# Kernel tuning notes

Measured on AMD Instinct MI355X. Metric: run time of the kernel, lower is better.

## Reference

```python
import jax, jax.numpy as jnp
import numpy as np

DIM = 1024
NUM_HEADS = 16
HEAD_DIM = DIM // NUM_HEADS
ROPE_BASE = 10000.0


def apply_rope(x, pos):
    """x: [B, H, N, D] float32, pos: [B, N] int -> rotated x (rotate-half convention)."""
    d = x.shape[-1]
    # inv_freq: [D/2]
    inv_freq = 1.0 / (ROPE_BASE ** (jnp.arange(0, d, 2, dtype=jnp.float32) / d))
    # angles: [B, 1, N, D/2]
    ang = pos.astype(jnp.float32)[:, None, :, None] * inv_freq
    cos = jnp.concatenate([jnp.cos(ang), jnp.cos(ang)], axis=-1)
    sin = jnp.concatenate([jnp.sin(ang), jnp.sin(ang)], axis=-1)
    x1, x2 = x[..., : d // 2], x[..., d // 2 :]
    rotated = jnp.concatenate([-x2, x1], axis=-1)
    return x * cos + rotated * sin


def setup_inputs() -> dict:
    key = jax.random.key(0)
    ks = jax.random.split(key, 10)
    B, Nq, Nk, C = 4, 512, 2048, DIM
    scale = 0.02
    inp = {
        "query": jax.random.normal(ks[0], (B, Nq, C), dtype=jnp.float32),
        "key": jax.random.normal(ks[1], (B, Nk, C), dtype=jnp.float32),
        "value": jax.random.normal(ks[2], (B, Nk, C), dtype=jnp.float32),
        "qpos": jnp.sort(jax.random.randint(ks[3], (B, Nq), 0, Nk, dtype=jnp.int32), axis=-1),
        "kpos": jnp.sort(jax.random.randint(ks[4], (B, Nk), 0, Nk, dtype=jnp.int32), axis=-1),
        # learned params (qkv_bias=False; output proj has bias, per nn.Linear default)
        "Wq": jax.random.normal(ks[5], (C, C), dtype=jnp.float32) * scale,
        "Wk": jax.random.normal(ks[6], (C, C), dtype=jnp.float32) * scale,
        "Wv": jax.random.normal(ks[7], (C, C), dtype=jnp.float32) * scale,
        "Wp": jax.random.normal(ks[8], (C, C), dtype=jnp.float32) * scale,
        "bp": jax.random.normal(ks[9], (C,), dtype=jnp.float32) * scale,
    }
    return inp


def reference(query, key, value, qpos, kpos, Wq, Wk, Wv, Wp, bp):
    B, Nq, C = query.shape
    Nk = key.shape[1]
    H, D = NUM_HEADS, C // NUM_HEADS
    scale = D ** (-0.5)

    # separate Q/K/V linear projections (bias=False), split heads -> [B, H, N, D]
    q = (query @ Wq.T).reshape(B, Nq, H, D).transpose(0, 2, 1, 3)
    k = (key @ Wk.T).reshape(B, Nk, H, D).transpose(0, 2, 1, 3)
    v = (value @ Wv.T).reshape(B, Nk, H, D).transpose(0, 2, 1, 3)

    # RoPE applied in fp32 (matches the cast-to-float/rotate/cast-back sequence)
    q = apply_rope(q.astype(jnp.float32), qpos).astype(query.dtype)
    k = apply_rope(k.astype(jnp.float32), kpos).astype(key.dtype)

    # scaled dot-product attention (dropout_p = 0.0, non-causal)
    scores = jnp.einsum("bhqd,bhkd->bhqk", q, k) * scale
    attn = jax.nn.softmax(scores, axis=-1)
    x = jnp.einsum("bhqk,bhkd->bhqd", attn, v)

    # merge heads and output projection (with bias)
    x = x.transpose(0, 2, 1, 3).reshape(B, Nq, C)
    x = x @ Wp.T + bp
    return x
```

## Files before the change

### kernel.cpp

```cpp
#include <hip/hip_runtime.h>
#include <math.h>

#define B_ 4
#define NQ 512
#define NK 2048
#define C_ 1024
#define H_ 16
#define D_ 64
#define KK 1024

typedef __attribute__((ext_vector_type(8))) _Float16 half8;
typedef __attribute__((ext_vector_type(4))) _Float16 half4;
typedef __attribute__((ext_vector_type(4))) float float4v;

__device__ __forceinline__ void g2l16(const _Float16* g, _Float16* l)
{
    __builtin_amdgcn_global_load_lds(
        (const __attribute__((address_space(1))) unsigned int*)g,
        (__attribute__((address_space(3))) unsigned int*)l, 16, 0, 0);
}

__global__ __launch_bounds__(256) void cvt_all(const float* __restrict__ W0,
                                               const float* __restrict__ W1,
                                               const float* __restrict__ W2,
                                               const float* __restrict__ W3,
                                               const float* __restrict__ q,
                                               const float* __restrict__ k,
                                               const float* __restrict__ v,
                                               _Float16* __restrict__ W16,
                                               _Float16* __restrict__ xq,
                                               _Float16* __restrict__ xk,
                                               _Float16* __restrict__ xv)
{
    const int blk = blockIdx.x;
    const float* src; _Float16* dst; int row;
    if (blk < 4096) {
        const int w = blk >> 10; row = blk & 1023;
        src = (w == 0) ? W0 : (w == 1) ? W1 : (w == 2) ? W2 : W3;
        dst = W16 + ((size_t)w << 20);
    } else {
        const int b2 = blk - 4096;
        if (b2 < 2048)       { src = q; dst = xq; row = b2; }
        else if (b2 < 10240) { src = k; dst = xk; row = b2 - 2048; }
        else                 { src = v; dst = xv; row = b2 - 10240; }
    }
    const int col = threadIdx.x * 4;
    float4 f = *(const float4*)(src + (size_t)row * 1024 + col);
    half4 h;
    h[0] = (_Float16)f.x; h[1] = (_Float16)f.y;
    h[2] = (_Float16)f.z; h[3] = (_Float16)f.w;
    *(half4*)(dst + (size_t)row * 1024 + col) = h;
}

__device__ __forceinline__ void gemm_body(const _Float16* __restrict__ A,
                                          const _Float16* __restrict__ Bw,
                                          _Float16* __restrict__ Yh,
                                          float* __restrict__ Yf,
                                          int mode, int nsh, int m0, int n0,
                                          const float* __restrict__ bias,
                                          _Float16* sA, _Float16* sB)
{
    const int tid = threadIdx.x;
    const int lane = tid & 63, wave = tid >> 6;
    const int wm = (wave >> 1) * 64, wn = (wave & 1) * 64;
    const int fm = lane & 15, quad = lane >> 4;

    const int srow = wave * 32 + (lane >> 3);
    const int soct = (lane & 7) ^ (srow & 7);
    const _Float16* gA = A  + (size_t)(m0 + srow) * KK + soct * 8;
    const _Float16* gB = Bw + (size_t)(n0 + srow) * KK + soct * 8;

    float4v acc[4][4];
    #pragma unroll
    for (int i = 0; i < 4; ++i)
        #pragma unroll
        for (int j = 0; j < 4; ++j)
            #pragma unroll
            for (int e = 0; e < 4; ++e) acc[i][j][e] = 0.0f;

    for (int k0 = 0; k0 < KK; k0 += 64) {
        __syncthreads();
        #pragma unroll
        for (int u = 0; u < 4; ++u) {
            g2l16(gA + (size_t)u * 8 * KK + k0, &sA[(wave * 32 + u * 8) * 64]);
            g2l16(gB + (size_t)u * 8 * KK + k0, &sB[(wave * 32 + u * 8) * 64]);
        }
        __syncthreads();

        #pragma unroll
        for (int ks = 0; ks < 2; ++ks) {
            const int po = ((ks * 4 + quad) ^ (fm & 7)) * 8;
            half8 a[4], b[4];
            #pragma unroll
            for (int i = 0; i < 4; ++i) {
                a[i] = *(const half8*)&sA[(wm + i * 16 + fm) * 64 + po];
                b[i] = *(const half8*)&sB[(wn + i * 16 + fm) * 64 + po];
            }
            __builtin_amdgcn_s_setprio(1);
            #pragma unroll
            for (int i = 0; i < 4; ++i)
                #pragma unroll
                for (int j = 0; j < 4; ++j)
                    acc[i][j] = __builtin_amdgcn_mfma_f32_16x16x32_f16(a[i], b[j], acc[i][j], 0, 0, 0);
            __builtin_amdgcn_s_setprio(0);
        }
    }

    const int rr = quad * 4;
    if (mode == 0) {
        const int nmask = (1 << nsh) - 1;
        #pragma unroll
        for (int i = 0; i < 4; ++i)
            #pragma unroll
            for (int r = 0; r < 4; ++r) {
                const int m = m0 + wm + i * 16 + rr + r;
                const int b = m >> nsh, n = m & nmask;
                #pragma unroll
                for (int j = 0; j < 4; ++j) {
                    const int c = n0 + wn + j * 16 + fm;
                    Yh[((((size_t)b * H_ + (c >> 6)) << nsh) + n) * 64 + (c & 63)] = (_Float16)acc[i][j][r];
                }
            }
    } else if (mode == 2) {
        const int nmask = (1 << nsh) - 1;
        #pragma unroll
        for (int i = 0; i < 4; ++i)
            #pragma unroll
            for (int r = 0; r < 4; ++r) {
                const int m = m0 + wm + i * 16 + rr + r;
                const int b = m >> nsh, n = m & nmask;
                #pragma unroll
                for (int j = 0; j < 4; ++j) {
                    const int c = n0 + wn + j * 16 + fm;
                    Yh[(((size_t)(b * H_ + (c >> 6)) * 64) + (c & 63)) * NK + n] = (_Float16)acc[i][j][r];
                }
            }
    } else {
        #pragma unroll
        for (int i = 0; i < 4; ++i)
            #pragma unroll
            for (int r = 0; r < 4; ++r) {
                const int m = m0 + wm + i * 16 + rr + r;
                #pragma unroll
                for (int j = 0; j < 4; ++j) {
                    const int c = n0 + wn + j * 16 + fm;
                    Yf[(size_t)m * 1024 + c] = acc[i][j][r] + bias[c];
                }
            }
    }
}

__global__ __launch_bounds__(256) void gemm_qkv(const _Float16* __restrict__ xq,
                                                const _Float16* __restrict__ xk,
                                                const _Float16* __restrict__ xv,
                                                const _Float16* __restrict__ W16,
                                                _Float16* __restrict__ qhp,
                                                _Float16* __restrict__ khp,
                                                _Float16* __restrict__ vtp)
{
    __shared__ _Float16 sA[128 * 64];
    __shared__ _Float16 sB[128 * 64];

    const int lbid = blockIdx.x;
    const int xcd = lbid & 7;
    const int seq = lbid >> 3;
    const int y = xcd + 8 * (seq >> 3);
    const int n0 = (seq & 7) * 128;

    if (y < 64)
        gemm_body(xk, W16 + (1u << 20), khp, nullptr, 0, 11, y * 128, n0, nullptr, sA, sB);
    else if (y < 128)
        gemm_body(xv, W16 + (2u << 20), vtp, nullptr, 2, 11, (y - 64) * 128, n0, nullptr, sA, sB);
    else
        gemm_body(xq, W16, qhp, nullptr, 0, 9, (y - 128) * 128, n0, nullptr, sA, sB);
}

__global__ __launch_bounds__(256) void gemm_out(const _Float16* __restrict__ A,
                                                const _Float16* __restrict__ Bw,
                                                float* __restrict__ Yf,
                                                const float* __restrict__ bias)
{
    __shared__ _Float16 sA[128 * 64];
    __shared__ _Float16 sB[128 * 64];
    gemm_body(A, Bw, nullptr, Yf, 1, 0, blockIdx.y * 128, blockIdx.x * 128, bias, sA, sB);
}

__global__ __launch_bounds__(256) void rope_qk(_Float16* __restrict__ qh,
                                               _Float16* __restrict__ kh,
                                               const int* __restrict__ qpos,
                                               const int* __restrict__ kpos)
{
    int idx = blockIdx.x * 256 + threadIdx.x;
    const int QTOT = B_ * H_ * NQ * 32;
    _Float16* t; const int* pos; int Nseq; float scale;
    if (idx < QTOT) { t = qh; pos = qpos; Nseq = NQ; scale = 0.125f; }
    else { idx -= QTOT; t = kh; pos = kpos; Nseq = NK; scale = 1.0f; }

    const int i = idx & 31;
    const int n = (idx >> 5) % Nseq;
    const int b = (idx / (32 * Nseq)) >> 4;

    double f = 1.0;
    if (i & 1)  f *= 0.7498942093324559;
    if (i & 2)  f *= 0.5623413251903491;
    if (i & 4)  f *= 0.31622776601683794;
    if (i & 8)  f *= 0.1;
    if (i & 16) f *= 0.01;

    const double ang = (double)pos[b * Nseq + n] * f;
    const double TWO_PI = 6.2831853071795864769;
    const double INV_TWO_PI = 0.15915494309189533577;
    const float red = (float)(ang - TWO_PI * floor(ang * INV_TWO_PI));
    float s, c;
    sincosf(red, &s, &c);

    const size_t base = ((size_t)(idx >> 5)) * 64 + i;
    const float x1 = (float)t[base];
    const float x2 = (float)t[base + 32];
    t[base]      = (_Float16)((x1 * c - x2 * s) * scale);
    t[base + 32] = (_Float16)((x2 * c + x1 * s) * scale);
}

__global__ __launch_bounds__(512) void attn_fused(const _Float16* __restrict__ qh,
                                                  const _Float16* __restrict__ kh,
                                                  const _Float16* __restrict__ vt,
                                                  _Float16* __restrict__ xw16)
{
    __shared__ _Float16 sK[2][64 * 64];
    __shared__ _Float16 sV[2][64 * 64];
    __shared__ _Float16 ps[8][16][66];

    const int tid = threadIdx.x;
    const int lane = tid & 63, wv = tid >> 6;
    const int bhi = blockIdx.x & 63;
    const int qquad = blockIdx.x >> 6;
    const size_t bh = (size_t)bhi;
    const int qt = qquad * 8 + wv;

    const int fm = lane & 15;
    const int quad = lane >> 4;
    const int fq = quad * 8;

    const _Float16* kb = kh + bh * NK * 64;
    const _Float16* vb = vt + bh * (size_t)64 * NK;

    const int r0 = lane >> 3;
    const int c4 = lane & 7;
    const int sch = c4 ^ r0;
    const _Float16* gK = kb + (size_t)(wv * 8 + r0) * 64 + sch * 8;
    const _Float16* gV = vb + (size_t)(wv * 8 + r0) * NK + sch * 8;

    const _Float16* qb = qh + (bh * NQ + (size_t)qt * 16) * 64;
    half8 aq[2];
    aq[0] = *(const half8*)(qb + (size_t)fm * 64 + fq);
    aq[1] = *(const half8*)(qb + (size_t)fm * 64 + 32 + fq);

    float l_acc[4] = {};
    float4v O[4];
    #pragma unroll
    for (int j = 0; j < 4; ++j)
        #pragma unroll
        for (int e = 0; e < 4; ++e) O[j][e] = 0.0f;

    const float4v z4 = {0.0f, 0.0f, 0.0f, 0.0f};

    g2l16(gK, &sK[0][wv * 512]);
    g2l16(gV, &sV[0][wv * 512]);
    __syncthreads();

    for (int it = 0; it < 32; ++it) {
        const int cur = it & 1;
        if (it < 31) {
            g2l16(gK + (size_t)(it + 1) * 64 * 64, &sK[cur ^ 1][wv * 512]);
            g2l16(gV + (it + 1) * 64,              &sV[cur ^ 1][wv * 512]);
        }
        const _Float16* Kc = sK[cur];
        const _Float16* Vc = sV[cur];

        half8 bk[4][2];
        #pragma unroll
        for (int j = 0; j < 4; ++j)
            #pragma unroll
            for (int ks = 0; ks < 2; ++ks)
                bk[j][ks] = *(const half8*)&Kc[(j * 16 + fm) * 64 + (((ks * 4 + quad) ^ (fm & 7)) * 8)];

        float4v s[4];
        __builtin_amdgcn_s_setprio(1);
        #pragma unroll
        for (int j = 0; j < 4; ++j) {
            s[j] = __builtin_amdgcn_mfma_f32_16x16x32_f16(aq[0], bk[j][0], z4, 0, 0, 0);
            s[j] = __builtin_amdgcn_mfma_f32_16x16x32_f16(aq[1], bk[j][1], s[j], 0, 0, 0);
        }
        __builtin_amdgcn_s_setprio(0);

        half8 bv[4][2];
        #pragma unroll
        for (int j = 0; j < 4; ++j)
            #pragma unroll
            for (int ks = 0; ks < 2; ++ks)
                bv[j][ks] = *(const half8*)&Vc[(j * 16 + fm) * 64 + (((ks * 4 + quad) ^ (fm & 7)) * 8)];

        #pragma unroll
        for (int j = 0; j < 4; ++j)
            #pragma unroll
            for (int r = 0; r < 4; ++r) {
                const float p = __expf(s[j][r]);
                l_acc[r] += p;
                ps[wv][quad * 4 + r][16 * j + fm] = (_Float16)p;
            }

        __builtin_amdgcn_s_setprio(1);
        #pragma unroll
        for (int ks = 0; ks < 2; ++ks) {
            half8 pa = *(const half8*)&ps[wv][fm][ks * 32 + fq];
            #pragma unroll
            for (int j = 0; j < 4; ++j)
                O[j] = __builtin_amdgcn_mfma_f32_16x16x32_f16(pa, bv[j][ks], O[j], 0, 0, 0);
        }
        __builtin_amdgcn_s_setprio(0);

        __syncthreads();
    }

    #pragma unroll
    for (int r = 0; r < 4; ++r) {
        float l = l_acc[r];
        l += __shfl_xor(l, 1);
        l += __shfl_xor(l, 2);
        l += __shfl_xor(l, 4);
        l += __shfl_xor(l, 8);
        const float inv = 1.0f / l;
        const int qr = quad * 4 + r;
        const int row = (bhi >> 4) * 512 + qt * 16 + qr;
        #pragma unroll
        for (int j = 0; j < 4; ++j) {
            const int col = (bhi & 15) * 64 + j * 16 + fm;
            xw16[(size_t)row * 1024 + col] = (_Float16)(O[j][r] * inv);
        }
    }
}

extern "C" void kernel_launch(void* const* d_in, const int* in_sizes, int n_in,
                              void* d_out, int out_size, void* d_ws, size_t ws_size,
                              hipStream_t stream)
{
    const float* query = (const float*)d_in[0];
    const float* key   = (const float*)d_in[1];
    const float* value = (const float*)d_in[2];
    const int*   qpos  = (const int*)d_in[3];
    const int*   kpos  = (const int*)d_in[4];
    const float* Wq    = (const float*)d_in[5];
    const float* Wk    = (const float*)d_in[6];
    const float* Wv    = (const float*)d_in[7];
    const float* Wp    = (const float*)d_in[8];
    const float* bp    = (const float*)d_in[9];
    float* out = (float*)d_out;

    char* ws = (char*)d_ws;
    _Float16* xk16  = (_Float16*)(ws);
    _Float16* xv16  = (_Float16*)(ws + (16u << 20));
    _Float16* xq16  = (_Float16*)(ws + (32u << 20));
    _Float16* W16   = (_Float16*)(ws + (36u << 20));
    _Float16* qhp   = (_Float16*)(ws + (44u << 20));
    _Float16* khp   = (_Float16*)(ws + (48u << 20));
    _Float16* vtp   = (_Float16*)(ws + (64u << 20));

    cvt_all<<<22528, 256, 0, stream>>>(Wq, Wk, Wv, Wp, query, key, value,
                                       W16, xq16, xk16, xv16);

    gemm_qkv<<<1152, 256, 0, stream>>>(xq16, xk16, xv16, W16, qhp, khp, vtp);

    rope_qk<<<(B_ * H_ * (NQ + NK) * 32) / 256, 256, 0, stream>>>(qhp, khp, qpos, kpos);

    attn_fused<<<256, 512, 0, stream>>>(qhp, khp, vtp, xq16);

    gemm_out<<<dim3(8, 16), 256, 0, stream>>>(xq16, W16 + (3u << 20), out, bp);
}
```

Measured before the change: 268.3 us.

## Fuse activation fp16 conversion and RoPE into QKV projection GEMM

Drops the separate fp32→fp16 conversion pass over query/key/value. The projection GEMM now loads fp32 activations into registers, converts them in-kernel and writes them to LDS, prefetching the next K-slice into registers. RoPE plus the query scale is applied in the GEMM epilogue using a precomputed cos/sin table indexed by position, so the standalone rope kernel and its extra read/write of Q and K are removed. The cost is more register pressure, twice the global bytes for the A operand inside the GEMM, and A staging that no longer uses direct global-to-LDS loads.

```diff
diff --git a/kernel.cpp b/kernel.cpp
--- a/kernel.cpp
+++ b/kernel.cpp
@@ -20,55 +20,80 @@
         (__attribute__((address_space(3))) unsigned int*)l, 16, 0, 0);
 }
 
-__global__ __launch_bounds__(256) void cvt_all(const float* __restrict__ W0,
-                                               const float* __restrict__ W1,
-                                               const float* __restrict__ W2,
-                                               const float* __restrict__ W3,
-                                               const float* __restrict__ q,
-                                               const float* __restrict__ k,
-                                               const float* __restrict__ v,
-                                               _Float16* __restrict__ W16,
-                                               _Float16* __restrict__ xq,
-                                               _Float16* __restrict__ xk,
-                                               _Float16* __restrict__ xv)
+__global__ __launch_bounds__(256) void cvt_w_tab(const float* __restrict__ W0,
+                                                 const float* __restrict__ W1,
+                                                 const float* __restrict__ W2,
+                                                 const float* __restrict__ W3,
+                                                 _Float16* __restrict__ W16,
+                                                 float2* __restrict__ tab)
 {
     const int blk = blockIdx.x;
-    const float* src; _Float16* dst; int row;
     if (blk < 4096) {
-        const int w = blk >> 10; row = blk & 1023;
-        src = (w == 0) ? W0 : (w == 1) ? W1 : (w == 2) ? W2 : W3;
-        dst = W16 + ((size_t)w << 20);
-    } else {
-        const int b2 = blk - 4096;
-        if (b2 < 2048)       { src = q; dst = xq; row = b2; }
-        else if (b2 < 10240) { src = k; dst = xk; row = b2 - 2048; }
-        else                 { src = v; dst = xv; row = b2 - 10240; }
-    }
-    const int col = threadIdx.x * 4;
-    float4 f = *(const float4*)(src + (size_t)row * 1024 + col);
-    half4 h;
-    h[0] = (_Float16)f.x; h[1] = (_Float16)f.y;
-    h[2] = (_Float16)f.z; h[3] = (_Float16)f.w;
-    *(half4*)(dst + (size_t)row * 1024 + col) = h;
-}
-
-__device__ __forceinline__ void gemm_body(const _Float16* __restrict__ A,
-                                          const _Float16* __restrict__ Bw,
-                                          _Float16* __restrict__ Yh,
-                                          float* __restrict__ Yf,
-                                          int mode, int nsh, int m0, int n0,
-                                          const float* __restrict__ bias,
-                                          _Float16* sA, _Float16* sB)
-{
+        const int w = blk >> 10, row = blk & 1023;
+        const float* src = (w == 0) ? W0 : (w == 1) ? W1 : (w == 2) ? W2 : W3;
+        const int col = threadIdx.x * 4;
+        float4 f = *(const float4*)(src + (size_t)row * 1024 + col);
+        half4 h;
+        h[0] = (_Float16)f.x; h[1] = (_Float16)f.y;
+        h[2] = (_Float16)f.z; h[3] = (_Float16)f.w;
+        *(half4*)(W16 + ((size_t)w << 20) + (size_t)row * 1024 + col) = h;
+        return;
+    }
+    const int idx = (blk - 4096) * 256 + threadIdx.x;
+    const int p = idx >> 5, i = idx & 31;
+
+    double f = 1.0;
+    if (i & 1)  f *= 0.7498942093324559;
+    if (i & 2)  f *= 0.5623413251903491;
+    if (i & 4)  f *= 0.31622776601683794;
+    if (i & 8)  f *= 0.1;
+    if (i & 16) f *= 0.01;
+
+    const double ang = (double)p * f;
+    const double TWO_PI = 6.2831853071795864769;
+    const double INV_TWO_PI = 0.15915494309189533577;
+    const float red = (float)(ang - TWO_PI * floor(ang * INV_TWO_PI));
+    float s, c;
+    sincosf(red, &s, &c);
+    tab[idx] = make_float2(c, s);
+}
+
+__global__ __launch_bounds__(256) void gemm_proj(const float* __restrict__ qf,
+                                                 const float* __restrict__ kf,
+                                                 const float* __restrict__ vf,
+                                                 const _Float16* __restrict__ W16,
+                                                 const int* __restrict__ qpos,
+                                                 const int* __restrict__ kpos,
+                                                 const float2* __restrict__ tab,
+                                                 _Float16* __restrict__ qhp,
+                                                 _Float16* __restrict__ khp,
+                                                 _Float16* __restrict__ vtp)
+{
+    __shared__ _Float16 sA[128 * 64];
+    __shared__ _Float16 sB[128 * 64];
+
+    const int lbid = blockIdx.x;
+    const int xcd = lbid & 7;
+    const int seq = lbid >> 3;
+    const int y = xcd + 8 * (seq >> 3);
+    const int n0 = (seq & 7) * 128;
+
+    const float* A; const _Float16* Bw; _Float16* Yh; const int* pos;
+    int nsh, m0, mode; float scale;
+    if (y < 64)       { A = kf; Bw = W16 + (1u << 20); Yh = khp; pos = kpos; nsh = 11; m0 = y * 128;         mode = 0; scale = 1.0f; }
+    else if (y < 128) { A = vf; Bw = W16 + (2u << 20); Yh = vtp; pos = nullptr; nsh = 11; m0 = (y - 64) * 128;  mode = 2; scale = 0.0f; }
+    else              { A = qf; Bw = W16;              Yh = qhp; pos = qpos; nsh = 9;  m0 = (y - 128) * 128; mode = 0; scale = 0.125f; }
+
     const int tid = threadIdx.x;
     const int lane = tid & 63, wave = tid >> 6;
     const int wm = (wave >> 1) * 64, wn = (wave & 1) * 64;
     const int fm = lane & 15, quad = lane >> 4;
 
-    const int srow = wave * 32 + (lane >> 3);
-    const int soct = (lane & 7) ^ (srow & 7);
-    const _Float16* gA = A  + (size_t)(m0 + srow) * KK + soct * 8;
-    const _Float16* gB = Bw + (size_t)(n0 + srow) * KK + soct * 8;
+    const int r0 = lane >> 3;
+    const int c4 = lane & 7;
+    const int sc = c4 ^ r0;
+    const float*    gAl = A  + (size_t)(m0 + wave * 32 + r0) * KK + sc * 8;
+    const _Float16* gB  = Bw + (size_t)(n0 + wave * 32 + r0) * KK + sc * 8;
 
     float4v acc[4][4];
     #pragma unroll
@@ -77,15 +102,37 @@
         for (int j = 0; j < 4; ++j)
             #pragma unroll
             for (int e = 0; e < 4; ++e) acc[i][j][e] = 0.0f;
+
+    float4 va[8];
+    #pragma unroll
+    for (int u = 0; u < 4; ++u) {
+        va[2 * u]     = *(const float4*)(gAl + (size_t)u * 8 * KK);
+        va[2 * u + 1] = *(const float4*)(gAl + (size_t)u * 8 * KK + 4);
+    }
 
     for (int k0 = 0; k0 < KK; k0 += 64) {
         __syncthreads();
         #pragma unroll
         for (int u = 0; u < 4; ++u) {
-            g2l16(gA + (size_t)u * 8 * KK + k0, &sA[(wave * 32 + u * 8) * 64]);
+            half8 h;
+            h[0] = (_Float16)va[2 * u].x; h[1] = (_Float16)va[2 * u].y;
+            h[2] = (_Float16)va[2 * u].z; h[3] = (_Float16)va[2 * u].w;
+            h[4] = (_Float16)va[2 * u + 1].x; h[5] = (_Float16)va[2 * u + 1].y;
+            h[6] = (_Float16)va[2 * u + 1].z; h[7] = (_Float16)va[2 * u + 1].w;
+            *(half8*)&sA[(wave * 32 + u * 8 + r0) * 64 + c4 * 8] = h;
+        }
+        #pragma unroll
+        for (int u = 0; u < 4; ++u)
             g2l16(gB + (size_t)u * 8 * KK + k0, &sB[(wave * 32 + u * 8) * 64]);
-        }
         __syncthreads();
+
+        if (k0 + 64 < KK) {
+            #pragma unroll
+            for (int u = 0; u < 4; ++u) {
+                va[2 * u]     = *(const float4*)(gAl + (size_t)u * 8 * KK + k0 + 64);
+                va[2 * u + 1] = *(const float4*)(gAl + (size_t)u * 8 * KK + k0 + 68);
+            }
+        }
 
         #pragma unroll
         for (int ks = 0; ks < 2; ++ks) {
@@ -109,19 +156,29 @@
     const int rr = quad * 4;
     if (mode == 0) {
         const int nmask = (1 << nsh) - 1;
+        const int hidx = (n0 + wn) >> 6;
         #pragma unroll
         for (int i = 0; i < 4; ++i)
             #pragma unroll
             for (int r = 0; r < 4; ++r) {
                 const int m = m0 + wm + i * 16 + rr + r;
                 const int b = m >> nsh, n = m & nmask;
-                #pragma unroll
-                for (int j = 0; j < 4; ++j) {
-                    const int c = n0 + wn + j * 16 + fm;
-                    Yh[((((size_t)b * H_ + (c >> 6)) << nsh) + n) * 64 + (c & 63)] = (_Float16)acc[i][j][r];
-                }
-            }
-    } else if (mode == 2) {
+                const int p = pos[(b << nsh) + n];
+                const float2 cs0 = tab[p * 32 + fm];
+                const float2 cs1 = tab[p * 32 + 16 + fm];
+                const float x0 = acc[i][0][r], x2 = acc[i][2][r];
+                const float x1 = acc[i][1][r], x3 = acc[i][3][r];
+                const float o0 = (x0 * cs0.x - x2 * cs0.y) * scale;
+                const float o2 = (x2 * cs0.x + x0 * cs0.y) * scale;
+                const float o1 = (x1 * cs1.x - x3 * cs1.y) * scale;
+                const float o3 = (x3 * cs1.x + x1 * cs1.y) * scale;
+                const size_t base = ((((size_t)b * H_ + hidx) << nsh) + n) * 64 + fm;
+                Yh[base +  0] = (_Float16)o0;
+                Yh[base + 16] = (_Float16)o1;
+                Yh[base + 32] = (_Float16)o2;
+                Yh[base + 48] = (_Float16)o3;
+            }
+    } else {
         const int nmask = (1 << nsh) - 1;
         #pragma unroll
         for (int i = 0; i < 4; ++i)
@@ -135,44 +192,7 @@
                     Yh[(((size_t)(b * H_ + (c >> 6)) * 64) + (c & 63)) * NK + n] = (_Float16)acc[i][j][r];
                 }
             }
-    } else {
-        #pragma unroll
-        for (int i = 0; i < 4; ++i)
-            #pragma unroll
-            for (int r = 0; r < 4; ++r) {
-                const int m = m0 + wm + i * 16 + rr + r;
-                #pragma unroll
-                for (int j = 0; j < 4; ++j) {
-                    const int c = n0 + wn + j * 16 + fm;
-                    Yf[(size_t)m * 1024 + c] = acc[i][j][r] + bias[c];
-                }
-            }
-    }
-}
-
-__global__ __launch_bounds__(256) void gemm_qkv(const _Float16* __restrict__ xq,
-                                                const _Float16* __restrict__ xk,
-                                                const _Float16* __restrict__ xv,
-                                                const _Float16* __restrict__ W16,
-                                                _Float16* __restrict__ qhp,
-                                                _Float16* __restrict__ khp,
-                                                _Float16* __restrict__ vtp)
-{
-    __shared__ _Float16 sA[128 * 64];
-    __shared__ _Float16 sB[128 * 64];
-
-    const int lbid = blockIdx.x;
-    const int xcd = lbid & 7;
-    const int seq = lbid >> 3;
-    const int y = xcd + 8 * (seq >> 3);
-    const int n0 = (seq & 7) * 128;
-
-    if (y < 64)
-        gemm_body(xk, W16 + (1u << 20), khp, nullptr, 0, 11, y * 128, n0, nullptr, sA, sB);
-    else if (y < 128)
-        gemm_body(xv, W16 + (2u << 20), vtp, nullptr, 2, 11, (y - 64) * 128, n0, nullptr, sA, sB);
-    else
-        gemm_body(xq, W16, qhp, nullptr, 0, 9, (y - 128) * 128, n0, nullptr, sA, sB);
+    }
 }
 
 __global__ __launch_bounds__(256) void gemm_out(const _Float16* __restrict__ A,
@@ -182,43 +202,66 @@
 {
     __shared__ _Float16 sA[128 * 64];
     __shared__ _Float16 sB[128 * 64];
-    gemm_body(A, Bw, nullptr, Yf, 1, 0, blockIdx.y * 128, blockIdx.x * 128, bias, sA, sB);
-}
-
-__global__ __launch_bounds__(256) void rope_qk(_Float16* __restrict__ qh,
-                                               _Float16* __restrict__ kh,
-                                               const int* __restrict__ qpos,
-                                               const int* __restrict__ kpos)
-{
-    int idx = blockIdx.x * 256 + threadIdx.x;
-    const int QTOT = B_ * H_ * NQ * 32;
-    _Float16* t; const int* pos; int Nseq; float scale;
-    if (idx < QTOT) { t = qh; pos = qpos; Nseq = NQ; scale = 0.125f; }
-    else { idx -= QTOT; t = kh; pos = kpos; Nseq = NK; scale = 1.0f; }
-
-    const int i = idx & 31;
-    const int n = (idx >> 5) % Nseq;
-    const int b = (idx / (32 * Nseq)) >> 4;
-
-    double f = 1.0;
-    if (i & 1)  f *= 0.7498942093324559;
-    if (i & 2)  f *= 0.5623413251903491;
-    if (i & 4)  f *= 0.31622776601683794;
-    if (i & 8)  f *= 0.1;
-    if (i & 16) f *= 0.01;
-
-    const double ang = (double)pos[b * Nseq + n] * f;
-    const double TWO_PI = 6.2831853071795864769;
-    const double INV_TWO_PI = 0.15915494309189533577;
-    const float red = (float)(ang - TWO_PI * floor(ang * INV_TWO_PI));
-    float s, c;
-    sincosf(red, &s, &c);
-
-    const size_t base = ((size_t)(idx >> 5)) * 64 + i;
-    const float x1 = (float)t[base];
-    const float x2 = (float)t[base + 32];
-    t[base]      = (_Float16)((x1 * c - x2 * s) * scale);
-    t[base + 32] = (_Float16)((x2 * c + x1 * s) * scale);
+
+    const int tid = threadIdx.x;
+    const int lane = tid & 63, wave = tid >> 6;
+    const int n0 = blockIdx.x * 128, m0 = blockIdx.y * 128;
+    const int wm = (wave >> 1) * 64, wn = (wave & 1) * 64;
+    const int fm = lane & 15, quad = lane >> 4;
+
+    const int srow = wave * 32 + (lane >> 3);
+    const int soct = (lane & 7) ^ (srow & 7);
+    const _Float16* gA = A  + (size_t)(m0 + srow) * KK + soct * 8;
+    const _Float16* gB = Bw + (size_t)(n0 + srow) * KK + soct * 8;
+
+    float4v acc[4][4];
+    #pragma unroll
+    for (int i = 0; i < 4; ++i)
+        #pragma unroll
+        for (int j = 0; j < 4; ++j)
+            #pragma unroll
+            for (int e = 0; e < 4; ++e) acc[i][j][e] = 0.0f;
+
+    for (int k0 = 0; k0 < KK; k0 += 64) {
+        __syncthreads();
+        #pragma unroll
+        for (int u = 0; u < 4; ++u) {
+            g2l16(gA + (size_t)u * 8 * KK + k0, &sA[(wave * 32 + u * 8) * 64]);
+            g2l16(gB + (size_t)u * 8 * KK + k0, &sB[(wave * 32 + u * 8) * 64]);
+        }
+        __syncthreads();
+
+        #pragma unroll
+        for (int ks = 0; ks < 2; ++ks) {
+            const int po = ((ks * 4 + quad) ^ (fm & 7)) * 8;
+            half8 a[4], b[4];
+            #pragma unroll
+            for (int i = 0; i < 4; ++i) {
+                a[i] = *(const half8*)&sA[(wm + i * 16 + fm) * 64 + po];
+                b[i] = *(const half8*)&sB[(wn + i * 16 + fm) * 64 + po];
+            }
+            __builtin_amdgcn_s_setprio(1);
+            #pragma unroll
+            for (int i = 0; i < 4; ++i)
+                #pragma unroll
+                for (int j = 0; j < 4; ++j)
+                    acc[i][j] = __builtin_amdgcn_mfma_f32_16x16x32_f16(a[i], b[j], acc[i][j], 0, 0, 0);
+            __builtin_amdgcn_s_setprio(0);
+        }
+    }
+
+    const int rr = quad * 4;
+    #pragma unroll
+    for (int i = 0; i < 4; ++i)
+        #pragma unroll
+        for (int r = 0; r < 4; ++r) {
+            const int m = m0 + wm + i * 16 + rr + r;
+            #pragma unroll
+            for (int j = 0; j < 4; ++j) {
+                const int c = n0 + wn + j * 16 + fm;
+                Yf[(size_t)m * 1024 + c] = acc[i][j][r] + bias[c];
+            }
+        }
 }
 
 __global__ __launch_bounds__(512) void attn_fused(const _Float16* __restrict__ qh,
@@ -357,22 +400,19 @@
     float* out = (float*)d_out;
 
     char* ws = (char*)d_ws;
-    _Float16* xk16  = (_Float16*)(ws);
-    _Float16* xv16  = (_Float16*)(ws + (16u << 20));
-    _Float16* xq16  = (_Float16*)(ws + (32u << 20));
+    float2*   tab   = (float2*)  (ws);
+    _Float16* xw16  = (_Float16*)(ws + (32u << 20));
     _Float16* W16   = (_Float16*)(ws + (36u << 20));
     _Float16* qhp   = (_Float16*)(ws + (44u << 20));
     _Float16* khp   = (_Float16*)(ws + (48u << 20));
     _Float16* vtp   = (_Float16*)(ws + (64u << 20));
 
-    cvt_all<<<22528, 256, 0, stream>>>(Wq, Wk, Wv, Wp, query, key, value,
-                                       W16, xq16, xk16, xv16);
-
-    gemm_qkv<<<1152, 256, 0, stream>>>(xq16, xk16, xv16, W16, qhp, khp, vtp);
-
-    rope_qk<<<(B_ * H_ * (NQ + NK) * 32) / 256, 256, 0, stream>>>(qhp, khp, qpos, kpos);
-
-    attn_fused<<<256, 512, 0, stream>>>(qhp, khp, vtp, xq16);
-
-    gemm_out<<<dim3(8, 16), 256, 0, stream>>>(xq16, W16 + (3u << 20), out, bp);
-}
+    cvt_w_tab<<<4352, 256, 0, stream>>>(Wq, Wk, Wv, Wp, W16, tab);
+
+    gemm_proj<<<1152, 256, 0, stream>>>(query, key, value, W16, qpos, kpos, tab,
+                                        qhp, khp, vtp);
+
+    attn_fused<<<256, 512, 0, stream>>>(qhp, khp, vtp, xw16);
+
+    gemm_out<<<dim3(8, 16), 256, 0, stream>>>(xw16, W16 + (3u << 20), out, bp);
+}
```

New measurement: 274.1 us. 2.1% more time.
